# Kernel tuning notes

Hardware: AMD Instinct MI355X
Metric: run time of the kernel (lower is better)

Reference implementation:

```python
import jax, jax.numpy as jnp
import numpy as np

B, S, D, H = 4, 2048, 1024, 16
HD = D // H  # head_dim = 64


def setup_inputs() -> dict:
    key = jax.random.key(0)
    ks = jax.random.split(key, 6)
    sd = 1.0 / np.sqrt(D)
    return {
        "x": jax.random.normal(ks[0], (B, S, D), dtype=jnp.float32),
        "y": jax.random.normal(ks[1], (B, S, D), dtype=jnp.float32),
        "mask": jax.random.normal(ks[2], (1, 1, S, S), dtype=jnp.float32),
        "Wkv": jax.random.normal(ks[3], (D, 2 * D), dtype=jnp.float32) * sd,
        "bkv": jnp.zeros((2 * D,), dtype=jnp.float32),
        "Wq": jax.random.normal(ks[4], (D, D), dtype=jnp.float32) * sd,
        "bq": jnp.zeros((D,), dtype=jnp.float32),
        "Wo": jax.random.normal(ks[5], (D, D), dtype=jnp.float32) * sd,
        "bo": jnp.zeros((D,), dtype=jnp.float32),
    }


def reference(x, y, mask, Wkv, bkv, Wq, bq, Wo, bo):
    b, s, d = x.shape
    kv = x @ Wkv + bkv                      # [B,S,2D]
    q = y @ Wq + bq                         # [B,S,D]
    kv = kv.reshape(b, s, H, 2 * HD).transpose(0, 2, 1, 3)  # [B,H,S,2HD]
    q = q.reshape(b, s, H, HD).transpose(0, 2, 1, 3)        # [B,H,S,HD]
    k, v = kv[..., :HD], kv[..., HD:]
    scaled = jnp.einsum("bhqd,bhkd->bhqk", q, k) / jnp.sqrt(jnp.float32(HD))
    scaled = scaled + mask                  # additive mask, broadcast [1,1,S,S]
    attn = jax.nn.softmax(scaled, axis=-1)
    vals = jnp.einsum("bhqk,bhkd->bhqd", attn, v)  # [B,H,S,HD]
    vals = vals.transpose(0, 2, 1, 3).reshape(b, s, d)
    return vals @ Wo + bo
```

## Files before the change

### kernel.cpp

```cpp
#include <hip/hip_runtime.h>

#define LOG2E 1.44269504088896340736f
#define QSCALE 0.18033688011112042f

typedef __attribute__((ext_vector_type(8))) short bf16x8;
typedef __attribute__((ext_vector_type(4))) float f32x4;

__device__ __forceinline__ unsigned short f2b(float f) {
  union { float f; unsigned int u; } x; x.f = f;
  return (unsigned short)((x.u + 0x8000u) >> 16);
}

__device__ __forceinline__ unsigned int pk_bf16(float a, float b) {
  union { float f; unsigned int u; } xa, xb; xa.f = a; xb.f = b;
  return __builtin_amdgcn_perm(xb.u + 0x8000u, xa.u + 0x8000u, 0x07060302);
}

__device__ __forceinline__ void gld_lds16(const void* g, void* l) {
  __builtin_amdgcn_global_load_lds((const __attribute__((address_space(1))) void*)g,
                                   (__attribute__((address_space(3))) void*)l,
                                   16, 0, 0);
}

__device__ __forceinline__ void wgbar() {
  asm volatile("" ::: "memory");
  __builtin_amdgcn_s_barrier();
  asm volatile("" ::: "memory");
}
#define SWAIT(s) asm volatile("s_waitcnt " s ::: "memory")

__global__ __launch_bounds__(256) void cast_xy(const float* __restrict__ x,
                                               const float* __restrict__ y,
                                               unsigned short* __restrict__ xb,
                                               unsigned short* __restrict__ yb) {
  int i = blockIdx.x * 256 + threadIdx.x;
  const float* in = x; unsigned short* out = xb;
  if (i >= 2097152) { in = y; out = yb; i -= 2097152; }
  float4 v = ((const float4*)in)[i];
  uint2 o;
  o.x = pk_bf16(v.x, v.y);
  o.y = pk_bf16(v.z, v.w);
  ((uint2*)out)[i] = o;
}

__global__ __launch_bounds__(256) void scale_mask(const float* __restrict__ in,
                                                  float* __restrict__ out) {
  int i = blockIdx.x * 256 + threadIdx.x;
  f32x4 v = ((const f32x4*)in)[i];
  ((f32x4*)out)[i] = v * LOG2E;
}

__global__ __launch_bounds__(256) void transpose_cast_all(
    const float* __restrict__ Wkv, const float* __restrict__ Wq,
    const float* __restrict__ Wo, unsigned short* __restrict__ wkvt,
    unsigned short* __restrict__ wqt, unsigned short* __restrict__ wot) {
  __shared__ float t[32][33];
  int tb = blockIdx.x;
  const float* W; unsigned short* Wt; int N;
  if (tb < 2048)      { W = Wkv; Wt = wkvt; N = 2048; }
  else if (tb < 3072) { W = Wq;  Wt = wqt;  N = 1024; tb -= 2048; }
  else                { W = Wo;  Wt = wot;  N = 1024; tb -= 3072; }
  const int K = 1024;
  int tilesN = N >> 5;
  int nb = (tb % tilesN) * 32, kb = (tb / tilesN) * 32;
  int j = threadIdx.x & 31, i0 = threadIdx.x >> 5;
  #pragma unroll
  for (int p = 0; p < 4; ++p) {
    int i = i0 + p * 8;
    t[i][j] = W[(size_t)(kb + i) * N + nb + j];
  }
  __syncthreads();
  #pragma unroll
  for (int p = 0; p < 4; ++p) {
    int i = i0 + p * 8;
    Wt[(size_t)(nb + i) * K + kb + j] = f2b(t[j][i]);
  }
}

template <int MODE>
__global__ __launch_bounds__(256)
void gemm128(const unsigned short* __restrict__ A,
             const unsigned short* __restrict__ Bt,
             const float* __restrict__ bias,
             void* __restrict__ out0, void* __restrict__ out1,
             int M, int N, int K) {
  __shared__ __align__(16) unsigned short As[128 * 64];
  __shared__ __align__(16) unsigned short Bs[128 * 64];
  const int tid = threadIdx.x;
  const int bn = blockIdx.x, bm = blockIdx.y;
  const int wave = tid >> 6, lane = tid & 63;
  const int wm = (wave >> 1) * 64, wn = (wave & 1) * 64;
  const int lrow = lane & 15, quad = lane >> 4;
  const int sw = lrow & 7;

  f32x4 acc[4][4];
  #pragma unroll
  for (int i = 0; i < 4; ++i)
    #pragma unroll
    for (int j = 0; j < 4; ++j)
      #pragma unroll
      for (int r = 0; r < 4; ++r) acc[i][j][r] = 0.f;

  const unsigned short* Ab = A + (size_t)(bm * 128) * K;
  const unsigned short* Bb = Bt + (size_t)(bn * 128) * K;

  for (int k0 = 0; k0 < K; k0 += 64) {
    #pragma unroll
    for (int i = 0; i < 4; ++i) {
      int e = i * 256 + tid;
      int row = e >> 3, gs = (e & 7) ^ (row & 7);
      gld_lds16(Ab + (size_t)row * K + k0 + gs * 8, &As[e * 8]);
    }
    #pragma unroll
    for (int i = 0; i < 4; ++i) {
      int e = i * 256 + tid;
      int row = e >> 3, gs = (e & 7) ^ (row & 7);
      gld_lds16(Bb + (size_t)row * K + k0 + gs * 8, &Bs[e * 8]);
    }
    __builtin_amdgcn_s_waitcnt(0);
    __syncthreads();
    #pragma unroll
    for (int ks = 0; ks < 2; ++ks) {
      bf16x8 af[4], bf[4];
      const int g = ((ks * 4 + quad) ^ sw) * 8;
      #pragma unroll
      for (int i = 0; i < 4; ++i)
        af[i] = *(const bf16x8*)&As[(wm + i * 16 + lrow) * 64 + g];
      #pragma unroll
      for (int j = 0; j < 4; ++j)
        bf[j] = *(const bf16x8*)&Bs[(wn + j * 16 + lrow) * 64 + g];
      #pragma unroll
      for (int i = 0; i < 4; ++i)
        #pragma unroll
        for (int j = 0; j < 4; ++j)
          acc[i][j] = __builtin_amdgcn_mfma_f32_16x16x32_bf16(af[i], bf[j], acc[i][j], 0, 0, 0);
    }
    __syncthreads();
  }

  const int col0 = bn * 128 + wn;
  #pragma unroll
  for (int i = 0; i < 4; ++i) {
    const int row0 = bm * 128 + wm + i * 16 + quad * 4;
    const int b = row0 >> 11, s0 = row0 & 2047;
    #pragma unroll
    for (int j = 0; j < 4; ++j) {
      const int cc = j * 16 + lrow;
      const float bv = bias[col0 + cc];
      float v0 = acc[i][j][0] + bv, v1 = acc[i][j][1] + bv;
      float v2 = acc[i][j][2] + bv, v3 = acc[i][j][3] + bv;
      if (MODE == 0) {
        float* C = (float*)out0;
        size_t off = (size_t)row0 * N + col0 + cc;
        C[off] = v0; C[off + N] = v1; C[off + 2 * N] = v2; C[off + 3 * N] = v3;
      } else if (MODE == 1) {
        const int h = col0 >> 7;
        if ((col0 & 64) == 0) {
          unsigned short* Kb = (unsigned short*)out0;
          size_t base = ((size_t)(b * 16 + h) * 2048 + s0) * 64 + cc;
          Kb[base] = f2b(v0); Kb[base + 64] = f2b(v1);
          Kb[base + 128] = f2b(v2); Kb[base + 192] = f2b(v3);
        } else {
          unsigned short* Vt = (unsigned short*)out1;
          size_t base = ((size_t)(b * 16 + h) * 64 + cc) * 2048 + s0;
          uint2 p; p.x = pk_bf16(v0, v1); p.y = pk_bf16(v2, v3);
          *(uint2*)&Vt[base] = p;
        }
      } else {
        v0 *= QSCALE; v1 *= QSCALE; v2 *= QSCALE; v3 *= QSCALE;
        const int h = col0 >> 6;
        unsigned short* Qb = (unsigned short*)out0;
        size_t base = ((size_t)(b * 16 + h) * 2048 + s0) * 64 + cc;
        Qb[base] = f2b(v0); Qb[base + 64] = f2b(v1);
        Qb[base + 128] = f2b(v2); Qb[base + 192] = f2b(v3);
      }
    }
  }
}

__global__ __launch_bounds__(256, 4)
void attn(const unsigned short* __restrict__ Qbuf,
          const unsigned short* __restrict__ Kbuf,
          const unsigned short* __restrict__ Vtbuf,
          const float* __restrict__ masks,
          unsigned short* __restrict__ vals) {
  const int blk = blockIdx.x;
  const int xcd = blk & 7, slot = blk >> 3;
  const int qt = xcd * 2 + (slot >> 6);
  const int hb = slot & 63;
  const int b = hb >> 4, h = hb & 15;
  const int tid = threadIdx.x, lane = tid & 63, w = tid >> 6;
  const int lrow = lane & 15, quad = lane >> 4;
  const int sw = lrow & 7;

  __shared__ __align__(16) unsigned short Ks[2][64 * 64];
  __shared__ __align__(16) unsigned short Vs[64 * 64];
  __shared__ __align__(16) unsigned short Ps[128 * 64];

  const unsigned short* qp = Qbuf + ((size_t)(b * 16 + h) * 2048 + qt * 128) * 64;
  const unsigned short* kp = Kbuf + (size_t)(b * 16 + h) * 2048 * 64;
  const unsigned short* vp = Vtbuf + (size_t)(b * 16 + h) * 64 * 2048;
  const float* mp = masks + (size_t)(qt * 128 + w * 32) * 2048;

  #pragma unroll
  for (int i = 0; i < 4; ++i) {
    int e = i * 256 + tid;
    int row = e >> 3, gs = (e & 7) ^ (row & 7);
    gld_lds16(qp + (size_t)row * 64 + gs * 8, &Ps[e * 8]);
  }
  #pragma unroll
  for (int i = 0; i < 2; ++i) {
    int e = i * 256 + tid;
    int row = e >> 3, gs = (e & 7) ^ (row & 7);
    gld_lds16(kp + (size_t)row * 64 + gs * 8, &Ks[0][e * 8]);
  }
  #pragma unroll
  for (int i = 0; i < 2; ++i) {
    int e = i * 256 + tid;
    int row = e >> 3, gs = (e & 7) ^ (row & 7);
    gld_lds16(vp + (size_t)row * 2048 + gs * 8, &Vs[e * 8]);
  }
  SWAIT("vmcnt(4)");
  wgbar();

  bf16x8 qf[2][2];
  #pragma unroll
  for (int iq = 0; iq < 2; ++iq)
    #pragma unroll
    for (int ks = 0; ks < 2; ++ks)
      qf[iq][ks] = *(const bf16x8*)&Ps[(w * 32 + iq * 16 + lrow) * 64 + ((ks * 4 + quad) ^ sw) * 8];

  f32x4 o_acc[4][2];
  #pragma unroll
  for (int id = 0; id < 4; ++id)
    #pragma unroll
    for (int iq = 0; iq < 2; ++iq)
      #pragma unroll
      for (int r = 0; r < 4; ++r) o_acc[id][iq][r] = 0.f;
  float lsum[2] = {0.f, 0.f};

  for (int t = 0; t < 32; ++t) {
    unsigned short* Kc = &Ks[t & 1][0];
    unsigned short* Kn = &Ks[(t + 1) & 1][0];
    const int ktn = (t + 1) & 31;

    f32x4 z[4][2];
    #pragma unroll
    for (int ik = 0; ik < 4; ++ik)
      #pragma unroll
      for (int iq = 0; iq < 2; ++iq)
        z[ik][iq] = *(const f32x4*)(mp + (size_t)(iq * 16 + lrow) * 2048 + t * 64 + ik * 16 + quad * 4);

    SWAIT("vmcnt(10)");
    wgbar();

    #pragma unroll
    for (int i = 0; i < 2; ++i) {
      int e = i * 256 + tid;
      int row = e >> 3, gs = (e & 7) ^ (row & 7);
      gld_lds16(kp + (size_t)(ktn * 64 + row) * 64 + gs * 8, &Kn[e * 8]);
    }

    #pragma unroll
    for (int ks = 0; ks < 2; ++ks) {
      bf16x8 kf[4];
      const int g = ((ks * 4 + quad) ^ sw) * 8;
      #pragma unroll
      for (int ik = 0; ik < 4; ++ik)
        kf[ik] = *(const bf16x8*)&Kc[(ik * 16 + lrow) * 64 + g];
      #pragma unroll
      for (int ik = 0; ik < 4; ++ik)
        #pragma unroll
        for (int iq = 0; iq < 2; ++iq)
          z[ik][iq] = __builtin_amdgcn_mfma_f32_16x16x32_bf16(kf[ik], qf[iq][ks], z[ik][iq], 0, 0, 0);
    }

    #pragma unroll
    for (int ik = 0; ik < 4; ++ik)
      #pragma unroll
      for (int iq = 0; iq < 2; ++iq) {
        float e0 = exp2f(z[ik][iq][0]), e1 = exp2f(z[ik][iq][1]);
        float e2 = exp2f(z[ik][iq][2]), e3 = exp2f(z[ik][iq][3]);
        lsum[iq] += (e0 + e1) + (e2 + e3);
        uint2 p;
        p.x = pk_bf16(e0, e1);
        p.y = pk_bf16(e2, e3);
        *(uint2*)&Ps[(w * 32 + iq * 16 + lrow) * 64 +
                     ((ik * 2 + (quad >> 1)) ^ sw) * 8 + (quad & 1) * 4] = p;
      }
    SWAIT("lgkmcnt(0)");
    wgbar();

    #pragma unroll
    for (int ks = 0; ks < 2; ++ks) {
      bf16x8 vf[4], pf[2];
      const int g = ((ks * 4 + quad) ^ sw) * 8;
      #pragma unroll
      for (int id = 0; id < 4; ++id)
        vf[id] = *(const bf16x8*)&Vs[(id * 16 + lrow) * 64 + g];
      #pragma unroll
      for (int iq = 0; iq < 2; ++iq)
        pf[iq] = *(const bf16x8*)&Ps[(w * 32 + iq * 16 + lrow) * 64 + g];
      #pragma unroll
      for (int id = 0; id < 4; ++id)
        #pragma unroll
        for (int iq = 0; iq < 2; ++iq)
          o_acc[id][iq] = __builtin_amdgcn_mfma_f32_16x16x32_bf16(vf[id], pf[iq], o_acc[id][iq], 0, 0, 0);
    }

    wgbar();

    #pragma unroll
    for (int i = 0; i < 2; ++i) {
      int e = i * 256 + tid;
      int row = e >> 3, gs = (e & 7) ^ (row & 7);
      gld_lds16(vp + (size_t)row * 2048 + ktn * 64 + gs * 8, &Vs[e * 8]);
    }
  }

  unsigned short* ob = vals + (size_t)(b * 2048 + qt * 128 + w * 32) * 1024 + h * 64;
  #pragma unroll
  for (int iq = 0; iq < 2; ++iq) {
    float s = lsum[iq];
    s += __shfl_xor(s, 16);
    s += __shfl_xor(s, 32);
    float inv = 1.f / s;
    #pragma unroll
    for (int id = 0; id < 4; ++id) {
      uint2 p;
      p.x = pk_bf16(o_acc[id][iq][0] * inv, o_acc[id][iq][1] * inv);
      p.y = pk_bf16(o_acc[id][iq][2] * inv, o_acc[id][iq][3] * inv);
      *(uint2*)&ob[(size_t)(iq * 16 + lrow) * 1024 + id * 16 + quad * 4] = p;
    }
  }
}

extern "C" void kernel_launch(void* const* d_in, const int* in_sizes, int n_in,
                              void* d_out, int out_size, void* d_ws, size_t ws_size,
                              hipStream_t stream) {
  const float* x    = (const float*)d_in[0];
  const float* y    = (const float*)d_in[1];
  const float* mask = (const float*)d_in[2];
  const float* Wkv  = (const float*)d_in[3];
  const float* bkv  = (const float*)d_in[4];
  const float* Wq   = (const float*)d_in[5];
  const float* bq   = (const float*)d_in[6];
  const float* Wo   = (const float*)d_in[7];
  const float* bo   = (const float*)d_in[8];

  char* ws = (char*)d_ws;
  unsigned short* xb    = (unsigned short*)(ws + ((size_t)0 << 20));
  unsigned short* yb    = (unsigned short*)(ws + ((size_t)16 << 20));
  unsigned short* wkvt  = (unsigned short*)(ws + ((size_t)32 << 20));
  unsigned short* wqt   = (unsigned short*)(ws + ((size_t)36 << 20));
  unsigned short* wot   = (unsigned short*)(ws + ((size_t)38 << 20));
  unsigned short* kbuf  = (unsigned short*)(ws + ((size_t)40 << 20));
  unsigned short* vtbuf = (unsigned short*)(ws + ((size_t)56 << 20));
  unsigned short* qbuf  = (unsigned short*)(ws + ((size_t)72 << 20));
  unsigned short* valsb = (unsigned short*)(ws + ((size_t)88 << 20));
  float*          masks = (float*)        (ws + ((size_t)108 << 20));

  cast_xy<<<16384, 256, 0, stream>>>(x, y, xb, yb);
  scale_mask<<<4096, 256, 0, stream>>>(mask, masks);
  transpose_cast_all<<<4096, 256, 0, stream>>>(Wkv, Wq, Wo, wkvt, wqt, wot);

  gemm128<1><<<dim3(16, 64), 256, 0, stream>>>(xb, wkvt, bkv, kbuf, vtbuf, 8192, 2048, 1024);
  gemm128<2><<<dim3(8, 64), 256, 0, stream>>>(yb, wqt, bq, qbuf, nullptr, 8192, 1024, 1024);
  attn<<<1024, 256, 0, stream>>>(qbuf, kbuf, vtbuf, masks, valsb);
  gemm128<0><<<dim3(8, 64), 256, 0, stream>>>(valsb, wot, bo, (float*)d_out, nullptr, 8192, 1024, 1024);
}
```

Before: 440.1 us.

## Prefetch next tile's mask, interleave QK MFMA with exp, drop a barrier

```diff
diff --git a/kernel.cpp b/kernel.cpp
--- a/kernel.cpp
+++ b/kernel.cpp
@@ -220,7 +220,14 @@
     int row = e >> 3, gs = (e & 7) ^ (row & 7);
     gld_lds16(vp + (size_t)row * 2048 + gs * 8, &Vs[e * 8]);
   }
-  SWAIT("vmcnt(4)");
+  f32x4 zm0[2][2], zm1[2][2];
+  #pragma unroll
+  for (int iq = 0; iq < 2; ++iq) {
+    const float* mrow = mp + (size_t)(iq * 16 + lrow) * 2048 + quad * 4;
+    zm0[0][iq] = *(const f32x4*)(mrow);
+    zm0[1][iq] = *(const f32x4*)(mrow + 16);
+  }
+  SWAIT("vmcnt(0)");
   wgbar();
 
   bf16x8 qf[2][2];
@@ -239,19 +246,12 @@
       for (int r = 0; r < 4; ++r) o_acc[id][iq][r] = 0.f;
   float lsum[2] = {0.f, 0.f};
 
-  for (int t = 0; t < 32; ++t) {
+  auto tile_body = [&](int t, f32x4 (&zc01)[2][2], f32x4 (&zn01)[2][2]) {
     unsigned short* Kc = &Ks[t & 1][0];
     unsigned short* Kn = &Ks[(t + 1) & 1][0];
     const int ktn = (t + 1) & 31;
 
-    f32x4 z[4][2];
-    #pragma unroll
-    for (int ik = 0; ik < 4; ++ik)
-      #pragma unroll
-      for (int iq = 0; iq < 2; ++iq)
-        z[ik][iq] = *(const f32x4*)(mp + (size_t)(iq * 16 + lrow) * 2048 + t * 64 + ik * 16 + quad * 4);
-
-    SWAIT("vmcnt(10)");
+    SWAIT("vmcnt(0)");
     wgbar();
 
     #pragma unroll
@@ -260,27 +260,28 @@
       int row = e >> 3, gs = (e & 7) ^ (row & 7);
       gld_lds16(kp + (size_t)(ktn * 64 + row) * 64 + gs * 8, &Kn[e * 8]);
     }
-
-    #pragma unroll
-    for (int ks = 0; ks < 2; ++ks) {
-      bf16x8 kf[4];
-      const int g = ((ks * 4 + quad) ^ sw) * 8;
-      #pragma unroll
-      for (int ik = 0; ik < 4; ++ik)
-        kf[ik] = *(const bf16x8*)&Kc[(ik * 16 + lrow) * 64 + g];
-      #pragma unroll
-      for (int ik = 0; ik < 4; ++ik)
-        #pragma unroll
-        for (int iq = 0; iq < 2; ++iq)
-          z[ik][iq] = __builtin_amdgcn_mfma_f32_16x16x32_bf16(kf[ik], qf[iq][ks], z[ik][iq], 0, 0, 0);
-    }
-
-    #pragma unroll
-    for (int ik = 0; ik < 4; ++ik)
+    f32x4 zc23[2][2];
+    #pragma unroll
+    for (int iq = 0; iq < 2; ++iq) {
+      const float* mrow = mp + (size_t)(iq * 16 + lrow) * 2048 + quad * 4;
+      zn01[0][iq] = *(const f32x4*)(mrow + ktn * 64);
+      zn01[1][iq] = *(const f32x4*)(mrow + ktn * 64 + 16);
+      zc23[0][iq] = *(const f32x4*)(mrow + t * 64 + 32);
+      zc23[1][iq] = *(const f32x4*)(mrow + t * 64 + 48);
+    }
+
+    #pragma unroll
+    for (int ik = 0; ik < 4; ++ik) {
+      const int krow = (ik * 16 + lrow) * 64;
+      bf16x8 kf0 = *(const bf16x8*)&Kc[krow + ((quad ^ sw) * 8)];
+      bf16x8 kf1 = *(const bf16x8*)&Kc[krow + (((4 + quad) ^ sw) * 8)];
       #pragma unroll
       for (int iq = 0; iq < 2; ++iq) {
-        float e0 = exp2f(z[ik][iq][0]), e1 = exp2f(z[ik][iq][1]);
-        float e2 = exp2f(z[ik][iq][2]), e3 = exp2f(z[ik][iq][3]);
+        f32x4 zz = (ik < 2) ? zc01[ik][iq] : zc23[ik - 2][iq];
+        zz = __builtin_amdgcn_mfma_f32_16x16x32_bf16(kf0, qf[iq][0], zz, 0, 0, 0);
+        zz = __builtin_amdgcn_mfma_f32_16x16x32_bf16(kf1, qf[iq][1], zz, 0, 0, 0);
+        float e0 = exp2f(zz[0]), e1 = exp2f(zz[1]);
+        float e2 = exp2f(zz[2]), e3 = exp2f(zz[3]);
         lsum[iq] += (e0 + e1) + (e2 + e3);
         uint2 p;
         p.x = pk_bf16(e0, e1);
@@ -288,8 +289,8 @@
         *(uint2*)&Ps[(w * 32 + iq * 16 + lrow) * 64 +
                      ((ik * 2 + (quad >> 1)) ^ sw) * 8 + (quad & 1) * 4] = p;
       }
+    }
     SWAIT("lgkmcnt(0)");
-    wgbar();
 
     #pragma unroll
     for (int ks = 0; ks < 2; ++ks) {
@@ -316,6 +317,11 @@
       int row = e >> 3, gs = (e & 7) ^ (row & 7);
       gld_lds16(vp + (size_t)row * 2048 + ktn * 64 + gs * 8, &Vs[e * 8]);
     }
+  };
+
+  for (int t = 0; t < 32; t += 2) {
+    tile_body(t, zm0, zm1);
+    tile_body(t + 1, zm1, zm0);
   }
 
   unsigned short* ob = vals + (size_t)(b * 2048 + qt * 128 + w * 32) * 1024 + h * 64;
```

After: 694.4 us. 1.58x slower.
